# Kernel optimization log

Hardware: AMD Instinct MI355X
Metric: run time of the kernel (lower is better)

The kernel has to match this reference:

```python
import jax, jax.numpy as jnp
import numpy as np

NUM_HEADS = 8


def _mab(Q, K, Wq, bq, Wk, bk, Wv, bv, Wo, bo):
    # MAB with ln=False, dropout=0 (eval). Scale is sqrt(dim_V), matching source.
    B, Lq, _ = Q.shape
    Lk = K.shape[1]
    Dv = Wq.shape[1]
    dh = Dv // NUM_HEADS
    q = (Q @ Wq + bq).reshape(B, Lq, NUM_HEADS, dh).transpose(0, 2, 1, 3)
    k = (K @ Wk + bk).reshape(B, Lk, NUM_HEADS, dh).transpose(0, 2, 1, 3)
    v = (K @ Wv + bv).reshape(B, Lk, NUM_HEADS, dh).transpose(0, 2, 1, 3)
    A = jax.nn.softmax(jnp.einsum('bhqd,bhkd->bhqk', q, k) / jnp.sqrt(jnp.float32(Dv)), axis=-1)
    O = (q + jnp.einsum('bhqk,bhkd->bhqd', A, v)).transpose(0, 2, 1, 3).reshape(B, Lq, Dv)
    return O + jax.nn.relu(O @ Wo + bo)


def _forward(x, adj, gin_W, gin_b, geW1, geb1, geW2, geb2,
             gnW1, gnb1, gnW2, gnb2, goW, gob, S,
             mWq, mbq, mWk, mbk, mWv, mbv, mWo, mbo, finW, finb):
    B, V, T, D = x.shape
    Hd = gin_W.shape[1]
    # --- GNN encoder (adj path) ---
    h = x.reshape(B, V, T * D) @ gin_W + gin_b            # [B,V,H]
    # edge_mlp first linear on cat([h_i,h_j]) == h@Wi (row) + h@Wj (col); avoids 2H concat
    Wi, Wj = geW1[:Hd], geW1[Hd:]
    pre = (h @ Wi)[:, :, None, :] + (h @ Wj)[:, None, :, :] + geb1   # [B,V,V,H]
    e = jax.nn.relu(jax.nn.relu(pre) @ geW2 + geb2)       # [B,V,V,H]
    agg = jnp.einsum('bijh,bij->bih', e, adj)             # mask * sum over j, fused
    node = jax.nn.relu(jax.nn.relu(agg @ gnW1 + gnb1) @ gnW2 + gnb2)
    enc = node @ goW + gob                                # [B,V,H]
    # --- decoder: PMA + SAB + SAB + Linear ---
    o = _mab(jnp.broadcast_to(S, (B,) + S.shape[1:]), enc,
             mWq[0], mbq[0], mWk[0], mbk[0], mWv[0], mbv[0], mWo[0], mbo[0])
    o = _mab(o, o, mWq[1], mbq[1], mWk[1], mbk[1], mWv[1], mbv[1], mWo[1], mbo[1])
    o = _mab(o, o, mWq[2], mbq[2], mWk[2], mbk[2], mWv[2], mbv[2], mWo[2], mbo[2])
    out = o @ finW + finb                                 # [B,num_slots,T*OD]
    return out.reshape(B, S.shape[1], T, finW.shape[1] // T)


def setup_inputs() -> dict:
    key = jax.random.key(0)
    ks = jax.random.split(key, 16)
    B, V, T, D = 4, 256, 12, 4
    H, NS, OD = 256, 16, 32

    def w(k, shape, s=0.02):
        return s * jax.random.normal(k, shape, jnp.float32)

    return {
        'x': jax.random.normal(ks[0], (B, V, T, D), jnp.float32),
        'adj': (jax.random.uniform(ks[1], (B, V, V)) > 0.5).astype(jnp.float32),
        'gin_W': w(ks[2], (T * D, H)), 'gin_b': jnp.zeros((H,), jnp.float32),
        'geW1': w(ks[3], (2 * H, H)), 'geb1': jnp.zeros((H,), jnp.float32),
        'geW2': w(ks[4], (H, H)), 'geb2': jnp.zeros((H,), jnp.float32),
        'gnW1': w(ks[5], (H, H)), 'gnb1': jnp.zeros((H,), jnp.float32),
        'gnW2': w(ks[6], (H, H)), 'gnb2': jnp.zeros((H,), jnp.float32),
        'goW': w(ks[7], (H, H)), 'gob': jnp.zeros((H,), jnp.float32),
        'S': w(ks[8], (1, NS, H), 0.05),
        'mWq': w(ks[9], (3, H, H)), 'mbq': jnp.zeros((3, H), jnp.float32),
        'mWk': w(ks[10], (3, H, H)), 'mbk': jnp.zeros((3, H), jnp.float32),
        'mWv': w(ks[11], (3, H, H)), 'mbv': jnp.zeros((3, H), jnp.float32),
        'mWo': w(ks[12], (3, H, H)), 'mbo': jnp.zeros((3, H), jnp.float32),
        'finW': w(ks[13], (H, T * OD)), 'finb': jnp.zeros((T * OD,), jnp.float32),
    }


def reference(x, adj, gin_W, gin_b, geW1, geb1, geW2, geb2,
              gnW1, gnb1, gnW2, gnb2, goW, gob, S,
              mWq, mbq, mWk, mbk, mWv, mbv, mWo, mbo, finW, finb):
    return _forward(x, adj, gin_W, gin_b, geW1, geb1, geW2, geb2,
                    gnW1, gnb1, gnW2, gnb2, goW, gob, S,
                    mWq, mbq, mWk, mbk, mWv, mbv, mWo, mbo, finW, finb)
```

## Files before the change

### kernel.cpp

```cpp
#include <hip/hip_runtime.h>
#include <hip/hip_bf16.h>

typedef unsigned short u16;
typedef __bf16 bf8v __attribute__((ext_vector_type(8)));
typedef float f4v __attribute__((ext_vector_type(4)));

__device__ __forceinline__ float b2f(u16 v) {
  union { unsigned u; float f; } x; x.u = ((unsigned)v) << 16; return x.f;
}
__device__ __forceinline__ u16 f2b(float f) {
  union { float f; unsigned u; } x; x.f = f;
  unsigned r = (x.u + 0x7FFFu + ((x.u >> 16) & 1u)) >> 16;
  return (u16)r;
}
__device__ __forceinline__ unsigned pkbf(float a, float b) {
  union { __hip_bfloat162 h; unsigned u; } c;
  c.h = __float22bfloat162_rn(make_float2(a, b));
  return c.u;
}
__device__ __forceinline__ void up2(unsigned u, float& lo, float& hi) {
  union { unsigned x; float f; } a, b;
  a.x = u << 16; b.x = u & 0xffff0000u; lo = a.f; hi = b.f;
}

#define NFRAG 18

struct PreArgs {
  const float* fsrc[NFRAG];
  u16* fdst[NFRAG];
  int fstride[NFRAG];
  int fbase[NFRAG + 1];
  int fragTiles, hBase, prepBid, q1Bid;
  const float *x, *ginW, *ginb;
  u16* h_bf;
  const float *mbk, *mbv, *mbq, *S, *mWq;
  float *bkv0, *bqkv1, *bqkv2;
  u16* q1b;
};

__global__ __launch_bounds__(256) void k_pre(PreArgs a) {
  __shared__ __align__(16) char smem[27648];
  const int bid = blockIdx.x, t = threadIdx.x;

  if (bid < a.fragTiles) {
    u16* ld = (u16*)smem;
    int j = 0;
    while (j + 1 < NFRAG && a.fbase[j + 1] <= bid) j++;
    const int localT = bid - a.fbase[j];
    const float* src = a.fsrc[j];
    const int Ns = a.fstride[j];
    const int n0 = localT * 16;
    {
      const float* s = src + (size_t)t * Ns + n0;
      const float4 v0 = ((const float4*)s)[0], v1 = ((const float4*)s)[1];
      const float4 v2 = ((const float4*)s)[2], v3 = ((const float4*)s)[3];
      unsigned* row = (unsigned*)(ld + t * 20);
      row[0] = pkbf(v0.x, v0.y); row[1] = pkbf(v0.z, v0.w);
      row[2] = pkbf(v1.x, v1.y); row[3] = pkbf(v1.z, v1.w);
      row[4] = pkbf(v2.x, v2.y); row[5] = pkbf(v2.z, v2.w);
      row[6] = pkbf(v3.x, v3.y); row[7] = pkbf(v3.z, v3.w);
    }
    __syncthreads();
    u16* dst = a.fdst[j] + (size_t)localT * 4096;
#pragma unroll
    for (int s2 = 0; s2 < 2; s2++) {
      const int o = t * 2 + s2, kt = o >> 6, lane = o & 63;
      const int nlo = lane & 15, bk = kt * 32 + ((lane >> 4) << 3);
      union { u16 h[8]; uint4 q; } pk;
#pragma unroll
      for (int j2 = 0; j2 < 8; j2++) pk.h[j2] = ld[(bk + j2) * 20 + nlo];
      *(uint4*)(dst + (size_t)(kt * 64 + lane) * 8) = pk.q;
    }
    return;
  }
  if (bid < a.prepBid) {
    float (*xs)[48] = (float (*)[48])(smem + 10240);
    const int row0 = (bid - a.hBase) * 4;
    if (t < 192) {
      const int rr = t / 48, k = t % 48;
      xs[rr][k] = a.x[(size_t)(row0 + rr) * 48 + k];
    }
    __syncthreads();
    const float bias = a.ginb[t];
    float acc[4] = {bias, bias, bias, bias};
    for (int k = 0; k < 48; k++) {
      const float w = a.ginW[(size_t)k * 256 + t];
#pragma unroll
      for (int rr = 0; rr < 4; rr++) acc[rr] += xs[rr][k] * w;
    }
#pragma unroll
    for (int rr = 0; rr < 4; rr++) a.h_bf[(size_t)(row0 + rr) * 256 + t] = f2b(acc[rr]);
    return;
  }
  if (bid == a.prepBid) {
    a.bkv0[t] = a.mbk[t]; a.bkv0[256 + t] = a.mbv[t];
    a.bqkv1[t] = a.mbq[256 + t]; a.bqkv1[256 + t] = a.mbk[256 + t]; a.bqkv1[512 + t] = a.mbv[256 + t];
    a.bqkv2[t] = a.mbq[512 + t]; a.bqkv2[256 + t] = a.mbk[512 + t]; a.bqkv2[512 + t] = a.mbv[512 + t];
    return;
  }
  if (bid == a.q1Bid) {
    float* Ss = (float*)(smem + 11264);
    for (int idx = t; idx < 4096; idx += 256) Ss[idx] = a.S[idx];
    __syncthreads();
    float acc[16];
#pragma unroll
    for (int r = 0; r < 16; r++) acc[r] = 0.f;
    for (int k = 0; k < 256; k++) {
      const float w = a.mWq[(size_t)k * 256 + t];
#pragma unroll
      for (int r = 0; r < 16; r++) acc[r] += Ss[r * 256 + k] * w;
    }
    const float bq = a.mbq[t];
#pragma unroll
    for (int r = 0; r < 16; r++) a.q1b[r * 256 + t] = f2b(acc[r] + bq);
    return;
  }
}

__global__ __launch_bounds__(256) void k_wiwj(
    const u16* __restrict__ h, const u16* __restrict__ frag,
    float* __restrict__ hWiF, u16* __restrict__ hWjB) {
  __shared__ __align__(16) u16 As[64 * 264];
  const int t = threadIdx.x, lane = t & 63, wv = t >> 6;
  const int m0 = blockIdx.x * 64, n0 = blockIdx.y * 128;
  {
    const int row = t >> 2, ch = t & 3;
#pragma unroll
    for (int s = 0; s < 8; s++)
      *(uint4*)(As + row * 264 + ch * 64 + s * 8) =
          *(const uint4*)(h + (size_t)(m0 + row) * 256 + ch * 64 + s * 8);
  }
  __syncthreads();
  f4v acc[4][2];
#pragma unroll
  for (int mt = 0; mt < 4; mt++)
#pragma unroll
    for (int nt = 0; nt < 2; nt++) acc[mt][nt] = (f4v){0.f, 0.f, 0.f, 0.f};
  const int Tw = (n0 >> 4) + wv * 2;
#pragma unroll
  for (int kt = 0; kt < 8; kt++) {
    bf8v af[4], bf[2];
#pragma unroll
    for (int mt = 0; mt < 4; mt++)
      af[mt] = *(const bf8v*)(As + (mt * 16 + (lane & 15)) * 264 + kt * 32 + ((lane >> 4) << 3));
#pragma unroll
    for (int nt = 0; nt < 2; nt++)
      bf[nt] = *(const bf8v*)(frag + ((size_t)((Tw + nt) * 8 + kt) * 64 + lane) * 8);
#pragma unroll
    for (int mt = 0; mt < 4; mt++)
#pragma unroll
      for (int nt = 0; nt < 2; nt++)
        acc[mt][nt] = __builtin_amdgcn_mfma_f32_16x16x32_bf16(af[mt], bf[nt], acc[mt][nt], 0, 0, 0);
  }
#pragma unroll
  for (int mt = 0; mt < 4; mt++)
#pragma unroll
    for (int nt = 0; nt < 2; nt++) {
      const int n = n0 + wv * 32 + nt * 16 + (lane & 15);
      const int mb = m0 + mt * 16 + ((lane >> 4) << 2);
#pragma unroll
      for (int r = 0; r < 4; r++) {
        if (n < 256)
          hWiF[(size_t)(mb + r) * 256 + n] = acc[mt][nt][r];
        else
          hWjB[(size_t)(mb + r) * 256 + (n - 256)] = f2b(acc[mt][nt][r]);
      }
    }
}

__global__ __launch_bounds__(256, 2) void k_edge(
    const float* __restrict__ hWiF, const u16* __restrict__ hWjB,
    const float* __restrict__ adj, const float* __restrict__ geb1,
    const u16* __restrict__ fragW2, const float* __restrict__ geb2,
    u16* __restrict__ aggB) {
  __shared__ __align__(16) u16 As[64 * 280];
  __shared__ float hi[256];
  __shared__ int jlist[256];
  __shared__ int cnt;
  const int t = threadIdx.x, lane = t & 63, wv = t >> 6;
  const int b = blockIdx.x >> 8, i = blockIdx.x & 255;
  if (t == 0) cnt = 0;
  __syncthreads();
  {
    const float a = adj[(size_t)(b * 256 + i) * 256 + t];
    hi[t] = hWiF[(size_t)(b * 256 + i) * 256 + t] + geb1[t];
    if (a != 0.f) { const int p = atomicAdd(&cnt, 1); jlist[p] = t; }
  }
  __syncthreads();
  const int nact = cnt;
  if (nact == 0) {
    if (lane < 16) {
#pragma unroll
      for (int nt = 0; nt < 4; nt++)
        aggB[(size_t)(b * 256 + i) * 256 + wv * 64 + nt * 16 + lane] = 0;
    }
    return;
  }
  const int nch = (nact + 63) >> 6;
  float bias2[4];
#pragma unroll
  for (int nt = 0; nt < 4; nt++) bias2[nt] = geb2[wv * 64 + nt * 16 + (lane & 15)];
  float aggAcc[4] = {0.f, 0.f, 0.f, 0.f};
  const u16* fw = fragW2 + lane * 8;

  for (int c = 0; c < nch; c++) {
    const int rows = min(64, nact - c * 64);
    {
      const int r = t >> 2, q = t & 3;
      const bool valid = (r < rows);
      const int j = valid ? jlist[c * 64 + r] : jlist[0];
      const uint4* s4 = (const uint4*)(hWjB + (size_t)(b * 256 + j) * 256 + q * 64);
      u16* dstrow = As + r * 280 + q * 72;
#pragma unroll
      for (int ii = 0; ii < 8; ii++) {
        const uint4 v = s4[ii];
        const int k = q * 64 + ii * 8;
        float f0, f1, f2, f3, f4, f5, f6, f7;
        up2(v.x, f0, f1); up2(v.y, f2, f3); up2(v.z, f4, f5); up2(v.w, f6, f7);
        uint4 qd;
        qd.x = pkbf(fmaxf(f0 + hi[k + 0], 0.f), fmaxf(f1 + hi[k + 1], 0.f));
        qd.y = pkbf(fmaxf(f2 + hi[k + 2], 0.f), fmaxf(f3 + hi[k + 3], 0.f));
        qd.z = pkbf(fmaxf(f4 + hi[k + 4], 0.f), fmaxf(f5 + hi[k + 5], 0.f));
        qd.w = pkbf(fmaxf(f6 + hi[k + 6], 0.f), fmaxf(f7 + hi[k + 7], 0.f));
        *(uint4*)(dstrow + ii * 8) = qd;
      }
    }
    __syncthreads();
    f4v acc[4][4];
#pragma unroll
    for (int jt = 0; jt < 4; jt++)
#pragma unroll
      for (int nt = 0; nt < 4; nt++) acc[jt][nt] = (f4v){0.f, 0.f, 0.f, 0.f};
    bf8v bcur[4];
#pragma unroll
    for (int nt = 0; nt < 4; nt++)
      bcur[nt] = *(const bf8v*)(fw + (size_t)((wv * 4 + nt) * 8 + 0) * 512);
#pragma unroll
    for (int kt = 0; kt < 8; kt++) {
      bf8v bnxt[4];
      if (kt < 7) {
#pragma unroll
        for (int nt = 0; nt < 4; nt++)
          bnxt[nt] = *(const bf8v*)(fw + (size_t)((wv * 4 + nt) * 8 + kt + 1) * 512);
      }
      bf8v af[4];
      const int coff = (kt >> 1) * 72 + (kt & 1) * 32 + ((lane >> 4) << 3);
#pragma unroll
      for (int jt = 0; jt < 4; jt++)
        af[jt] = *(const bf8v*)(As + (jt * 16 + (lane & 15)) * 280 + coff);
#pragma unroll
      for (int nt = 0; nt < 4; nt++)
#pragma unroll
        for (int jt = 0; jt < 4; jt++)
          acc[jt][nt] = __builtin_amdgcn_mfma_f32_16x16x32_bf16(af[jt], bcur[nt], acc[jt][nt], 0, 0, 0);
      if (kt < 7) {
#pragma unroll
        for (int nt = 0; nt < 4; nt++) bcur[nt] = bnxt[nt];
      }
    }
    const int rbase = (lane >> 4) * 4;
#pragma unroll
    for (int nt = 0; nt < 4; nt++) {
      float s = 0.f;
#pragma unroll
      for (int jt = 0; jt < 4; jt++) {
        const int r0 = jt * 16 + rbase;
#pragma unroll
        for (int r = 0; r < 4; r++) {
          const float e = fmaxf(acc[jt][nt][r] + bias2[nt], 0.f);
          s += (r0 + r < rows) ? e : 0.f;
        }
      }
      s += __shfl_xor(s, 16);
      s += __shfl_xor(s, 32);
      aggAcc[nt] += s;
    }
    __syncthreads();
  }
  if (lane < 16) {
#pragma unroll
    for (int nt = 0; nt < 4; nt++) {
      const int n = wv * 64 + nt * 16 + lane;
      aggB[(size_t)(b * 256 + i) * 256 + n] = f2b(aggAcc[nt]);
    }
  }
}


__device__ void g16(const u16* Al, const u16* __restrict__ frag,
                    const float* bias, int relu, u16* Ol, int t) {
  const int lane = t & 63, wv = t >> 6;
  f4v acc[2];
  acc[0] = (f4v){0.f, 0.f, 0.f, 0.f};
  acc[1] = (f4v){0.f, 0.f, 0.f, 0.f};
  const u16* abase = Al + (lane & 15) * 264 + ((lane >> 4) << 3);
  const u16* f0 = frag + ((size_t)((wv * 2 + 0) * 8) * 64 + lane) * 8;
  const u16* f1 = frag + ((size_t)((wv * 2 + 1) * 8) * 64 + lane) * 8;
  bf8v bc0 = *(const bf8v*)f0;
  bf8v bc1 = *(const bf8v*)f1;
#pragma unroll
  for (int kt = 0; kt < 8; kt++) {
    bf8v bn0, bn1;
    if (kt < 7) {
      bn0 = *(const bf8v*)(f0 + (size_t)(kt + 1) * 512);
      bn1 = *(const bf8v*)(f1 + (size_t)(kt + 1) * 512);
    }
    const bf8v af = *(const bf8v*)(abase + kt * 32);
    acc[0] = __builtin_amdgcn_mfma_f32_16x16x32_bf16(af, bc0, acc[0], 0, 0, 0);
    acc[1] = __builtin_amdgcn_mfma_f32_16x16x32_bf16(af, bc1, acc[1], 0, 0, 0);
    if (kt < 7) { bc0 = bn0; bc1 = bn1; }
  }
#pragma unroll
  for (int nt = 0; nt < 2; nt++) {
    const int col = (wv * 2 + nt) * 16 + (lane & 15);
    const float bv = bias[col];
#pragma unroll
    for (int r = 0; r < 4; r++) {
      const int row = ((lane >> 4) << 2) + r;
      float v = acc[nt][r] + bv;
      if (relu) v = fmaxf(v, 0.f);
      Ol[row * 264 + col] = f2b(v);
    }
  }
}

__device__ void g16kv(const u16* Al, const u16* __restrict__ frag,
                      const float* bias, u16* outG, int t) {
  const int lane = t & 63, wv = t >> 6;
  f4v acc[4];
#pragma unroll
  for (int nt = 0; nt < 4; nt++) acc[nt] = (f4v){0.f, 0.f, 0.f, 0.f};
  const u16* abase = Al + (lane & 15) * 264 + ((lane >> 4) << 3);
  const u16* fb[4];
#pragma unroll
  for (int nt = 0; nt < 4; nt++)
    fb[nt] = frag + ((size_t)((wv * 4 + nt) * 8) * 64 + lane) * 8;
  bf8v bc[4];
#pragma unroll
  for (int nt = 0; nt < 4; nt++) bc[nt] = *(const bf8v*)fb[nt];
#pragma unroll
  for (int kt = 0; kt < 8; kt++) {
    bf8v bn[4];
    if (kt < 7) {
#pragma unroll
      for (int nt = 0; nt < 4; nt++)
        bn[nt] = *(const bf8v*)(fb[nt] + (size_t)(kt + 1) * 512);
    }
    const bf8v af = *(const bf8v*)(abase + kt * 32);
#pragma unroll
    for (int nt = 0; nt < 4; nt++)
      acc[nt] = __builtin_amdgcn_mfma_f32_16x16x32_bf16(af, bc[nt], acc[nt], 0, 0, 0);
    if (kt < 7) {
#pragma unroll
      for (int nt = 0; nt < 4; nt++) bc[nt] = bn[nt];
    }
  }
#pragma unroll
  for (int nt = 0; nt < 4; nt++) {
    const int col = (wv * 4 + nt) * 16 + (lane & 15);
    const float bv = bias[col];
#pragma unroll
    for (int r = 0; r < 4; r++) {
      const int row = ((lane >> 4) << 2) + r;
      outG[(size_t)row * 512 + col] = f2b(acc[nt][r] + bv);
    }
  }
}

__device__ void attn_tile(const u16* __restrict__ qbuf,
                          const u16* __restrict__ kbuf, const u16* __restrict__ vbuf,
                          float* __restrict__ oF, u16* __restrict__ oB,
                          int b, int hd, float* qs, float* sc, float* vs, int t) {
  const int lane = t & 63, wv = t >> 6;
  const int Lk = 256;
  if (t < 64) {
    const int row = t >> 2, part = t & 3;
    const uint4 q4 = *(const uint4*)(qbuf + (size_t)row * 256 + hd * 32 + part * 8);
    float f0, f1, f2, f3, f4, f5, f6, f7;
    up2(q4.x, f0, f1); up2(q4.y, f2, f3); up2(q4.z, f4, f5); up2(q4.w, f6, f7);
    float4* d = (float4*)(qs + row * 32 + part * 8);
    d[0] = make_float4(f0, f1, f2, f3);
    d[1] = make_float4(f4, f5, f6, f7);
  }
  __syncthreads();
  {
    float kv[32];
    const uint4* kp = (const uint4*)(kbuf + (size_t)(b * Lk + t) * 512 + hd * 32);
#pragma unroll
    for (int c4 = 0; c4 < 4; c4++) {
      const uint4 k4 = kp[c4];
      up2(k4.x, kv[c4 * 8 + 0], kv[c4 * 8 + 1]);
      up2(k4.y, kv[c4 * 8 + 2], kv[c4 * 8 + 3]);
      up2(k4.z, kv[c4 * 8 + 4], kv[c4 * 8 + 5]);
      up2(k4.w, kv[c4 * 8 + 6], kv[c4 * 8 + 7]);
    }
    for (int r = 0; r < 16; r++) {
      float s = 0.f;
#pragma unroll
      for (int d = 0; d < 32; d++) s += qs[r * 32 + d] * kv[d];
      sc[r * 256 + t] = s * 0.0625f;
    }
  }
  __syncthreads();
  for (int r = wv * 4; r < wv * 4 + 4; r++) {
    float v[4];
    float mx = -1e30f;
#pragma unroll
    for (int q2 = 0; q2 < 4; q2++) {
      v[q2] = sc[r * 256 + lane + q2 * 64];
      mx = fmaxf(mx, v[q2]);
    }
    for (int off = 32; off; off >>= 1) mx = fmaxf(mx, __shfl_xor(mx, off));
    float sum = 0.f;
#pragma unroll
    for (int q2 = 0; q2 < 4; q2++) { v[q2] = __expf(v[q2] - mx); sum += v[q2]; }
    for (int off = 32; off; off >>= 1) sum += __shfl_xor(sum, off);
    const float inv = 1.f / sum;
#pragma unroll
    for (int q2 = 0; q2 < 4; q2++) sc[r * 256 + lane + q2 * 64] = v[q2] * inv;
  }
  __syncthreads();
  for (int u = t; u < 1024; u += 256) {
    const int row = u >> 2, part = u & 3;
    const uint4 v4 = *(const uint4*)(vbuf + (size_t)(b * Lk + row) * 512 + hd * 32 + part * 8);
    float f0, f1, f2, f3, f4, f5, f6, f7;
    up2(v4.x, f0, f1); up2(v4.y, f2, f3); up2(v4.z, f4, f5); up2(v4.w, f6, f7);
    float4* d = (float4*)(vs + row * 32 + part * 8);
    d[0] = make_float4(f0, f1, f2, f3);
    d[1] = make_float4(f4, f5, f6, f7);
  }
  __syncthreads();
  const int r0 = t >> 5, d = t & 31;
  float a0 = qs[r0 * 32 + d], a1 = qs[(r0 + 8) * 32 + d];
#pragma unroll 4
  for (int j = 0; j < Lk; j++) {
    const float vv = vs[j * 32 + d];
    a0 += sc[r0 * 256 + j] * vv;
    a1 += sc[(r0 + 8) * 256 + j] * vv;
  }
  const int c0 = hd * 32 + d;
  oF[(size_t)(b * 16 + r0) * 256 + c0] = a0;
  oB[(size_t)(b * 16 + r0) * 256 + c0] = f2b(a0);
  oF[(size_t)(b * 16 + r0 + 8) * 256 + c0] = a1;
  oB[(size_t)(b * 16 + r0 + 8) * 256 + c0] = f2b(a1);
}

__device__ void wprojG(const u16* __restrict__ o1b, const float* __restrict__ o1f,
                       const u16* __restrict__ frag, const float* __restrict__ bias,
                       u16* actL, float* residL, int b, int T, int lane) {
  f4v acc = (f4v){0.f, 0.f, 0.f, 0.f};
  const u16* abase = o1b + (size_t)(b * 16 + (lane & 15)) * 256 + ((lane >> 4) << 3);
  const u16* fbase = frag + ((size_t)(T * 8) * 64 + lane) * 8;
#pragma unroll
  for (int kt = 0; kt < 8; kt++)
    acc = __builtin_amdgcn_mfma_f32_16x16x32_bf16(*(const bf8v*)(abase + kt * 32),
                                                  *(const bf8v*)(fbase + (size_t)kt * 512), acc, 0, 0, 0);
  const int col = T * 16 + (lane & 15);
  const float bv = bias[col];
#pragma unroll
  for (int r = 0; r < 4; r++) {
    const int row = ((lane >> 4) << 2) + r;
    const float v = fmaxf(acc[r] + bv, 0.f) + o1f[(size_t)(b * 16 + row) * 256 + col];
    residL[row * 256 + col] = v;
    actL[row * 264 + col] = f2b(v);
  }
}

template <int NT>
__device__ __forceinline__ void wprojQn(
    const u16* actL, const u16* __restrict__ frag,
    const float* __restrict__ bias, u16* qkvL, int T0, int lane) {
  f4v acc[NT];
#pragma unroll
  for (int nt = 0; nt < NT; nt++) acc[nt] = (f4v){0.f, 0.f, 0.f, 0.f};
  const u16* abase = actL + (lane & 15) * 264 + ((lane >> 4) << 3);
#pragma unroll
  for (int kt = 0; kt < 8; kt++) {
    const bf8v af = *(const bf8v*)(abase + kt * 32);
#pragma unroll
    for (int nt = 0; nt < NT; nt++) {
      const bf8v bf = *(const bf8v*)(frag + ((size_t)((T0 + nt) * 8 + kt) * 64 + lane) * 8);
      acc[nt] = __builtin_amdgcn_mfma_f32_16x16x32_bf16(af, bf, acc[nt], 0, 0, 0);
    }
  }
#pragma unroll
  for (int nt = 0; nt < NT; nt++) {
    const int col = (T0 + nt) * 16 + (lane & 15);
    const float bv = bias[col];
#pragma unroll
    for (int r = 0; r < 4; r++) {
      const int row = ((lane >> 4) << 2) + r;
      qkvL[row * 776 + col] = f2b(acc[nt][r] + bv);
    }
  }
}

__device__ void wprojR(const u16* actIn, const u16* __restrict__ frag,
                       const float* __restrict__ bias, u16* actOut, float* residL,
                       int T, int lane) {
  f4v acc = (f4v){0.f, 0.f, 0.f, 0.f};
  const u16* abase = actIn + (lane & 15) * 264 + ((lane >> 4) << 3);
  const u16* fbase = frag + ((size_t)(T * 8) * 64 + lane) * 8;
#pragma unroll
  for (int kt = 0; kt < 8; kt++)
    acc = __builtin_amdgcn_mfma_f32_16x16x32_bf16(*(const bf8v*)(abase + kt * 32),
                                                  *(const bf8v*)(fbase + (size_t)kt * 512), acc, 0, 0, 0);
  const int col = T * 16 + (lane & 15);
  const float bv = bias[col];
#pragma unroll
  for (int r = 0; r < 4; r++) {
    const int row = ((lane >> 4) << 2) + r;
    const float v = fmaxf(acc[r] + bv, 0.f) + residL[row * 256 + col];
    residL[row * 256 + col] = v;
    actOut[row * 264 + col] = f2b(v);
  }
}

__device__ void wprojF(const u16* actL, const u16* __restrict__ frag,
                       const float* __restrict__ bias, float* __restrict__ outG,
                       int T, int lane) {
  f4v acc = (f4v){0.f, 0.f, 0.f, 0.f};
  const u16* abase = actL + (lane & 15) * 264 + ((lane >> 4) << 3);
  const u16* fbase = frag + ((size_t)(T * 8) * 64 + lane) * 8;
#pragma unroll
  for (int kt = 0; kt < 8; kt++)
    acc = __builtin_amdgcn_mfma_f32_16x16x32_bf16(*(const bf8v*)(abase + kt * 32),
                                                  *(const bf8v*)(fbase + (size_t)kt * 512), acc, 0, 0, 0);
  const int col = T * 16 + (lane & 15);
  const float bv = bias[col];
#pragma unroll
  for (int r = 0; r < 4; r++) {
    const int row = ((lane >> 4) << 2) + r;
    outG[(size_t)row * 384 + col] = acc[r] + bv;
  }
}

__device__ void attnB(const u16* qkvL, float* residL, u16* actOut, float* ps,
                      int hd, int lane) {
  const int r = lane & 15, cg = lane >> 4;
  float qv[32];
  {
    const uint4* qp = (const uint4*)(qkvL + r * 776 + hd * 32);
#pragma unroll
    for (int c4 = 0; c4 < 4; c4++) {
      const uint4 q4 = qp[c4];
      up2(q4.x, qv[c4 * 8 + 0], qv[c4 * 8 + 1]);
      up2(q4.y, qv[c4 * 8 + 2], qv[c4 * 8 + 3]);
      up2(q4.z, qv[c4 * 8 + 4], qv[c4 * 8 + 5]);
      up2(q4.w, qv[c4 * 8 + 6], qv[c4 * 8 + 7]);
    }
  }
  float p[4];
#pragma unroll
  for (int c = 0; c < 4; c++) {
    const int cc = cg * 4 + c;
    const uint4* kp = (const uint4*)(qkvL + cc * 776 + 256 + hd * 32);
    float s = 0.f;
#pragma unroll
    for (int c4 = 0; c4 < 4; c4++) {
      const uint4 k4 = kp[c4];
      float k0, k1;
      up2(k4.x, k0, k1); s += qv[c4 * 8 + 0] * k0 + qv[c4 * 8 + 1] * k1;
      up2(k4.y, k0, k1); s += qv[c4 * 8 + 2] * k0 + qv[c4 * 8 + 3] * k1;
      up2(k4.z, k0, k1); s += qv[c4 * 8 + 4] * k0 + qv[c4 * 8 + 5] * k1;
      up2(k4.w, k0, k1); s += qv[c4 * 8 + 6] * k0 + qv[c4 * 8 + 7] * k1;
    }
    p[c] = s * 0.0625f;
  }
  float mx = fmaxf(fmaxf(p[0], p[1]), fmaxf(p[2], p[3]));
  mx = fmaxf(mx, __shfl_xor(mx, 16));
  mx = fmaxf(mx, __shfl_xor(mx, 32));
  float sum = 0.f;
#pragma unroll
  for (int c = 0; c < 4; c++) { p[c] = __expf(p[c] - mx); sum += p[c]; }
  sum += __shfl_xor(sum, 16);
  sum += __shfl_xor(sum, 32);
  const float inv = 1.f / sum;
#pragma unroll
  for (int c = 0; c < 4; c++) ps[r * 16 + cg * 4 + c] = p[c] * inv;
  float o[8];
#pragma unroll
  for (int j = 0; j < 8; j++) o[j] = qv[cg * 8 + j];
#pragma unroll
  for (int c = 0; c < 16; c++) {
    const float pv = ps[r * 16 + c];
    const uint4 v4 = *(const uint4*)(qkvL + c * 776 + 512 + hd * 32 + cg * 8);
    float v0, v1;
    up2(v4.x, v0, v1); o[0] += pv * v0; o[1] += pv * v1;
    up2(v4.y, v0, v1); o[2] += pv * v0; o[3] += pv * v1;
    up2(v4.z, v0, v1); o[4] += pv * v0; o[5] += pv * v1;
    up2(v4.w, v0, v1); o[6] += pv * v0; o[7] += pv * v1;
  }
  const int col0 = hd * 32 + cg * 8;
#pragma unroll
  for (int j = 0; j < 8; j++) residL[r * 256 + col0 + j] = o[j];
  unsigned* ob = (unsigned*)(actOut + r * 264 + col0);
  ob[0] = pkbf(o[0], o[1]); ob[1] = pkbf(o[2], o[3]);
  ob[2] = pkbf(o[4], o[5]); ob[3] = pkbf(o[6], o[7]);
}

struct TailArgs {
  const u16 *agg, *fGn1, *fGn2, *fGo, *fKV0, *fQKV1, *fQKV2, *fO0, *fO1, *fO2, *fFin, *q1b;
  const float *gnb1, *gnb2, *gob, *bkv0, *bqkv1, *bqkv2, *mbo, *finb;
  u16 *kv1, *o1b;
  float *o1f, *outF;
};

__global__ __launch_bounds__(512) void k_tail1(TailArgs a) {
  __shared__ __align__(16) u16 actA[16 * 264];
  __shared__ __align__(16) u16 actB[16 * 264];
  const int bid = blockIdx.x, t = threadIdx.x;
  const int r0 = bid * 16;
  {
    const int row = t >> 5, ch = t & 31;
    *(uint4*)(actA + row * 264 + ch * 8) =
        *(const uint4*)(a.agg + (size_t)(r0 + row) * 256 + ch * 8);
  }
  __syncthreads();
  g16(actA, a.fGn1, a.gnb1, 1, actB, t); __syncthreads();
  g16(actB, a.fGn2, a.gnb2, 1, actA, t); __syncthreads();
  g16(actA, a.fGo, a.gob, 0, actB, t); __syncthreads();
  g16kv(actB, a.fKV0, a.bkv0, a.kv1 + (size_t)r0 * 512, t);
}

__global__ __launch_bounds__(256) void k_tail2(TailArgs a) {
  __shared__ __align__(16) char smem[51200];
  float* qs = (float*)smem;
  float* sc = (float*)(smem + 2048);
  float* vs = (float*)(smem + 18432);
  attn_tile(a.q1b, a.kv1, a.kv1 + 256, a.o1f, a.o1b,
            (int)(blockIdx.x >> 3), (int)(blockIdx.x & 7), qs, sc, vs, (int)threadIdx.x);
}

__global__ __launch_bounds__(1024, 1) void k_tailB(TailArgs a) {
  __shared__ __align__(16) char smem[58112];
  const int t = threadIdx.x, lane = t & 63, w = t >> 6;
  const int b = blockIdx.x;
  u16* act0 = (u16*)smem;
  u16* act1 = (u16*)(smem + 8448);
  u16* qkvL = (u16*)(smem + 16896);
  float* residL = (float*)(smem + 41728);
  float* psL = (float*)smem;

  wprojG(a.o1b, a.o1f, a.fO0, a.mbo, act0, residL, b, w, lane);
  __syncthreads();
  wprojQn<3>(act0, a.fQKV1, a.bqkv1, qkvL, w * 3, lane);
  __syncthreads();
  if (w < 8) attnB(qkvL, residL, act1, psL + w * 256, w, lane);
  __syncthreads();
  wprojR(act1, a.fO1, a.mbo + 256, act0, residL, w, lane);
  __syncthreads();
  wprojQn<3>(act0, a.fQKV2, a.bqkv2, qkvL, w * 3, lane);
  __syncthreads();
  if (w < 8) attnB(qkvL, residL, act1, psL + w * 256, w, lane);
  __syncthreads();
  wprojR(act1, a.fO2, a.mbo + 512, act0, residL, w, lane);
  __syncthreads();
  for (int T = w; T < 24; T += 16)
    wprojF(act0, a.fFin, a.finb, a.outF + (size_t)b * 16 * 384, T, lane);
}

extern "C" void kernel_launch(void* const* d_in, const int* in_sizes, int n_in,
                              void* d_out, int out_size, void* d_ws, size_t ws_size,
                              hipStream_t stream) {
  const float* x    = (const float*)d_in[0];
  const float* adj  = (const float*)d_in[1];
  const float* ginW = (const float*)d_in[2];
  const float* ginb = (const float*)d_in[3];
  const float* geW1 = (const float*)d_in[4];
  const float* geb1 = (const float*)d_in[5];
  const float* geW2 = (const float*)d_in[6];
  const float* geb2 = (const float*)d_in[7];
  const float* gnW1 = (const float*)d_in[8];
  const float* gnb1 = (const float*)d_in[9];
  const float* gnW2 = (const float*)d_in[10];
  const float* gnb2 = (const float*)d_in[11];
  const float* goW  = (const float*)d_in[12];
  const float* gob  = (const float*)d_in[13];
  const float* S    = (const float*)d_in[14];
  const float* mWq  = (const float*)d_in[15];
  const float* mbq  = (const float*)d_in[16];
  const float* mWk  = (const float*)d_in[17];
  const float* mbk  = (const float*)d_in[18];
  const float* mWv  = (const float*)d_in[19];
  const float* mbv  = (const float*)d_in[20];
  const float* mWo  = (const float*)d_in[21];
  const float* mbo  = (const float*)d_in[22];
  const float* finW = (const float*)d_in[23];
  const float* finb = (const float*)d_in[24];
  (void)in_sizes; (void)n_in; (void)out_size; (void)ws_size;

  char* wp = (char*)d_ws;
  size_t off = 0;
  auto alloc = [&](size_t bytes) -> char* {
    char* p = wp + off;
    off += (bytes + 255) & ~(size_t)255;
    return p;
  };
  u16* h_bf     = (u16*)alloc(1024 * 256 * 2);
  float* hWiF   = (float*)alloc((size_t)1024 * 256 * 4);
  u16* hWjB     = (u16*)alloc(1024 * 256 * 2);
  u16* fWiWj    = (u16*)alloc(512 * 256 * 2);
  u16* fW2      = (u16*)alloc(256 * 256 * 2);
  u16* fGn1     = (u16*)alloc(256 * 256 * 2);
  u16* fGn2     = (u16*)alloc(256 * 256 * 2);
  u16* fGo      = (u16*)alloc(256 * 256 * 2);
  u16* fKV0     = (u16*)alloc(512 * 256 * 2);
  u16* fQKV1    = (u16*)alloc(768 * 256 * 2);
  u16* fQKV2    = (u16*)alloc(768 * 256 * 2);
  u16* fO0      = (u16*)alloc(256 * 256 * 2);
  u16* fO1      = (u16*)alloc(256 * 256 * 2);
  u16* fO2      = (u16*)alloc(256 * 256 * 2);
  u16* fFin     = (u16*)alloc(384 * 256 * 2);
  float* bkv0   = (float*)alloc(512 * 4);
  float* bqkv1  = (float*)alloc(768 * 4);
  float* bqkv2  = (float*)alloc(768 * 4);
  u16* q1b      = (u16*)alloc(16 * 256 * 2);
  u16* agg_b    = (u16*)alloc(1024 * 256 * 2);
  u16* kv1      = (u16*)alloc(1024 * 512 * 2);
  float* o1f    = (float*)alloc(64 * 256 * 4);
  u16* o1b      = (u16*)alloc(64 * 256 * 2);

  PreArgs P{};
  int nj = 0, tiles = 0;
  auto addF = [&](const float* s, int stride, u16* d, int nT) {
    P.fsrc[nj] = s; P.fdst[nj] = d; P.fstride[nj] = stride; P.fbase[nj] = tiles;
    tiles += nT; nj++;
  };
  addF(geW1, 256, fWiWj, 16);
  addF(geW1 + 65536, 256, fWiWj + 16 * 4096, 16);
  addF(geW2, 256, fW2, 16);
  addF(gnW1, 256, fGn1, 16);
  addF(gnW2, 256, fGn2, 16);
  addF(goW, 256, fGo, 16);
  addF(mWk, 256, fKV0, 16);
  addF(mWv, 256, fKV0 + 16 * 4096, 16);
  addF(mWq + 65536, 256, fQKV1, 16);
  addF(mWk + 65536, 256, fQKV1 + 16 * 4096, 16);
  addF(mWv + 65536, 256, fQKV1 + 32 * 4096, 16);
  addF(mWq + 131072, 256, fQKV2, 16);
  addF(mWk + 131072, 256, fQKV2 + 16 * 4096, 16);
  addF(mWv + 131072, 256, fQKV2 + 32 * 4096, 16);
  addF(mWo, 256, fO0, 16);
  addF(mWo + 65536, 256, fO1, 16);
  addF(mWo + 131072, 256, fO2, 16);
  addF(finW, 384, fFin, 24);
  P.fbase[nj] = tiles;
  P.fragTiles = tiles;
  P.hBase = tiles;
  P.prepBid = tiles + 256;
  P.q1Bid = tiles + 257;
  P.x = x; P.ginW = ginW; P.ginb = ginb; P.h_bf = h_bf;
  P.mbk = mbk; P.mbv = mbv; P.mbq = mbq; P.S = S; P.mWq = mWq;
  P.bkv0 = bkv0; P.bqkv1 = bqkv1; P.bqkv2 = bqkv2; P.q1b = q1b;

  TailArgs T{};
  T.agg = agg_b; T.fGn1 = fGn1; T.fGn2 = fGn2; T.fGo = fGo; T.fKV0 = fKV0;
  T.fQKV1 = fQKV1; T.fQKV2 = fQKV2; T.fO0 = fO0; T.fO1 = fO1; T.fO2 = fO2;
  T.fFin = fFin; T.q1b = q1b;
  T.gnb1 = gnb1; T.gnb2 = gnb2; T.gob = gob;
  T.bkv0 = bkv0; T.bqkv1 = bqkv1; T.bqkv2 = bqkv2; T.mbo = mbo; T.finb = finb;
  T.kv1 = kv1; T.o1b = o1b; T.o1f = o1f; T.outF = (float*)d_out;

  k_pre<<<dim3(tiles + 258), dim3(256), 0, stream>>>(P);
  k_wiwj<<<dim3(16, 4), dim3(256), 0, stream>>>(h_bf, fWiWj, hWiF, hWjB);
  k_edge<<<dim3(1024), dim3(256), 0, stream>>>(hWiF, hWjB, adj, geb1, fW2, geb2, agg_b);
  k_tail1<<<dim3(64), dim3(512), 0, stream>>>(T);
  k_tail2<<<dim3(32), dim3(256), 0, stream>>>(T);
  k_tailB<<<dim3(4), dim3(1024), 0, stream>>>(T);
}
```

Baseline: 220.8 us.

## Fuse three tail kernels into one persistent kernel with grid barriers

Merges the tail1, tail2 and tailB kernels into a single 64-block, 1024-thread kernel. Software grid barriers on a global atomic counter, reset in k_pre, separate the phases. Each phase's work is redistributed across 16 waves: single-tile GEMMs per wave and one attention row per wave. This removes two kernel launch gaps and their tail latency, but adds atomic spin barriers, relies on all 64 blocks being co-resident, and leaves most blocks idle in the later phases.

```diff
diff --git a/kernel.cpp b/kernel.cpp
--- a/kernel.cpp
+++ b/kernel.cpp
@@ -24,6 +24,7 @@
 }
 
 #define NFRAG 18
+#define TBLK 64
 
 struct PreArgs {
   const float* fsrc[NFRAG];
@@ -36,6 +37,7 @@
   const float *mbk, *mbv, *mbq, *S, *mWq;
   float *bkv0, *bqkv1, *bqkv2;
   u16* q1b;
+  int* bar;
 };
 
 __global__ __launch_bounds__(256) void k_pre(PreArgs a) {
@@ -93,6 +95,7 @@
     return;
   }
   if (bid == a.prepBid) {
+    if (t < 64) a.bar[t] = 0;
     a.bkv0[t] = a.mbk[t]; a.bkv0[256 + t] = a.mbv[t];
     a.bqkv1[t] = a.mbq[256 + t]; a.bqkv1[256 + t] = a.mbk[256 + t]; a.bqkv1[512 + t] = a.mbv[256 + t];
     a.bqkv2[t] = a.mbq[512 + t]; a.bqkv2[256 + t] = a.mbk[512 + t]; a.bqkv2[512 + t] = a.mbv[512 + t];
@@ -286,16 +289,55 @@
   }
 }
 
-
-__device__ void g16(const u16* Al, const u16* __restrict__ frag,
-                    const float* bias, int relu, u16* Ol, int t) {
-  const int lane = t & 63, wv = t >> 6;
+__device__ __forceinline__ void gridbar(int* cnt, int gen) {
+  __syncthreads();
+  if (threadIdx.x == 0) {
+    __hip_atomic_fetch_add(cnt, 1, __ATOMIC_RELEASE, __HIP_MEMORY_SCOPE_AGENT);
+    int it = 0;
+    while (__hip_atomic_load(cnt, __ATOMIC_ACQUIRE, __HIP_MEMORY_SCOPE_AGENT) < TBLK * gen) {
+      __builtin_amdgcn_s_sleep(8);
+      if (((++it) & 255) == 0)
+        __hip_atomic_fetch_add(cnt, 0, __ATOMIC_ACQ_REL, __HIP_MEMORY_SCOPE_AGENT);
+    }
+  }
+  __syncthreads();
+}
+
+__device__ void g16w(const u16* Al, const u16* __restrict__ frag,
+                     const float* bias, int relu, u16* Ol, int t) {
+  const int lane = t & 63, w = t >> 6;
+  f4v acc = (f4v){0.f, 0.f, 0.f, 0.f};
+  const u16* abase = Al + (lane & 15) * 264 + ((lane >> 4) << 3);
+  const u16* fb = frag + ((size_t)(w * 8) * 64 + lane) * 8;
+  bf8v bc = *(const bf8v*)fb;
+#pragma unroll
+  for (int kt = 0; kt < 8; kt++) {
+    bf8v bn;
+    if (kt < 7) bn = *(const bf8v*)(fb + (size_t)(kt + 1) * 512);
+    const bf8v af = *(const bf8v*)(abase + kt * 32);
+    acc = __builtin_amdgcn_mfma_f32_16x16x32_bf16(af, bc, acc, 0, 0, 0);
+    if (kt < 7) bc = bn;
+  }
+  const int col = w * 16 + (lane & 15);
+  const float bv = bias[col];
+#pragma unroll
+  for (int r = 0; r < 4; r++) {
+    const int row = ((lane >> 4) << 2) + r;
+    float v = acc[r] + bv;
+    if (relu) v = fmaxf(v, 0.f);
+    Ol[row * 264 + col] = f2b(v);
+  }
+}
+
+__device__ void g16kv2(const u16* Al, const u16* __restrict__ frag,
+                       const float* bias, u16* outG, int t) {
+  const int lane = t & 63, w = t >> 6;
   f4v acc[2];
   acc[0] = (f4v){0.f, 0.f, 0.f, 0.f};
   acc[1] = (f4v){0.f, 0.f, 0.f, 0.f};
   const u16* abase = Al + (lane & 15) * 264 + ((lane >> 4) << 3);
-  const u16* f0 = frag + ((size_t)((wv * 2 + 0) * 8) * 64 + lane) * 8;
-  const u16* f1 = frag + ((size_t)((wv * 2 + 1) * 8) * 64 + lane) * 8;
+  const u16* f0 = frag + ((size_t)((w * 2 + 0) * 8) * 64 + lane) * 8;
+  const u16* f1 = frag + ((size_t)((w * 2 + 1) * 8) * 64 + lane) * 8;
   bf8v bc0 = *(const bf8v*)f0;
   bf8v bc1 = *(const bf8v*)f1;
 #pragma unroll
@@ -312,52 +354,7 @@
   }
 #pragma unroll
   for (int nt = 0; nt < 2; nt++) {
-    const int col = (wv * 2 + nt) * 16 + (lane & 15);
-    const float bv = bias[col];
-#pragma unroll
-    for (int r = 0; r < 4; r++) {
-      const int row = ((lane >> 4) << 2) + r;
-      float v = acc[nt][r] + bv;
-      if (relu) v = fmaxf(v, 0.f);
-      Ol[row * 264 + col] = f2b(v);
-    }
-  }
-}
-
-__device__ void g16kv(const u16* Al, const u16* __restrict__ frag,
-                      const float* bias, u16* outG, int t) {
-  const int lane = t & 63, wv = t >> 6;
-  f4v acc[4];
-#pragma unroll
-  for (int nt = 0; nt < 4; nt++) acc[nt] = (f4v){0.f, 0.f, 0.f, 0.f};
-  const u16* abase = Al + (lane & 15) * 264 + ((lane >> 4) << 3);
-  const u16* fb[4];
-#pragma unroll
-  for (int nt = 0; nt < 4; nt++)
-    fb[nt] = frag + ((size_t)((wv * 4 + nt) * 8) * 64 + lane) * 8;
-  bf8v bc[4];
-#pragma unroll
-  for (int nt = 0; nt < 4; nt++) bc[nt] = *(const bf8v*)fb[nt];
-#pragma unroll
-  for (int kt = 0; kt < 8; kt++) {
-    bf8v bn[4];
-    if (kt < 7) {
-#pragma unroll
-      for (int nt = 0; nt < 4; nt++)
-        bn[nt] = *(const bf8v*)(fb[nt] + (size_t)(kt + 1) * 512);
-    }
-    const bf8v af = *(const bf8v*)(abase + kt * 32);
-#pragma unroll
-    for (int nt = 0; nt < 4; nt++)
-      acc[nt] = __builtin_amdgcn_mfma_f32_16x16x32_bf16(af, bc[nt], acc[nt], 0, 0, 0);
-    if (kt < 7) {
-#pragma unroll
-      for (int nt = 0; nt < 4; nt++) bc[nt] = bn[nt];
-    }
-  }
-#pragma unroll
-  for (int nt = 0; nt < 4; nt++) {
-    const int col = (wv * 4 + nt) * 16 + (lane & 15);
+    const int col = (w * 2 + nt) * 16 + (lane & 15);
     const float bv = bias[col];
 #pragma unroll
     for (int r = 0; r < 4; r++) {
@@ -367,11 +364,11 @@
   }
 }
 
-__device__ void attn_tile(const u16* __restrict__ qbuf,
-                          const u16* __restrict__ kbuf, const u16* __restrict__ vbuf,
-                          float* __restrict__ oF, u16* __restrict__ oB,
-                          int b, int hd, float* qs, float* sc, float* vs, int t) {
-  const int lane = t & 63, wv = t >> 6;
+__device__ void attn_tile_1024(const u16* __restrict__ qbuf,
+                               const u16* __restrict__ kbuf, const u16* __restrict__ vbuf,
+                               float* __restrict__ oF, u16* __restrict__ oB,
+                               int b, int hd, float* qs, float* sc, float* vs, int t) {
+  const int lane = t & 63, w = t >> 6;
   const int Lk = 256;
   if (t < 64) {
     const int row = t >> 2, part = t & 3;
@@ -383,7 +380,7 @@
     d[1] = make_float4(f4, f5, f6, f7);
   }
   __syncthreads();
-  {
+  if (t < 256) {
     float kv[32];
     const uint4* kp = (const uint4*)(kbuf + (size_t)(b * Lk + t) * 512 + hd * 32);
 #pragma unroll
@@ -402,7 +399,8 @@
     }
   }
   __syncthreads();
-  for (int r = wv * 4; r < wv * 4 + 4; r++) {
+  {
+    const int r = w;
     float v[4];
     float mx = -1e30f;
 #pragma unroll
@@ -420,8 +418,8 @@
     for (int q2 = 0; q2 < 4; q2++) sc[r * 256 + lane + q2 * 64] = v[q2] * inv;
   }
   __syncthreads();
-  for (int u = t; u < 1024; u += 256) {
-    const int row = u >> 2, part = u & 3;
+  {
+    const int row = t >> 2, part = t & 3;
     const uint4 v4 = *(const uint4*)(vbuf + (size_t)(b * Lk + row) * 512 + hd * 32 + part * 8);
     float f0, f1, f2, f3, f4, f5, f6, f7;
     up2(v4.x, f0, f1); up2(v4.y, f2, f3); up2(v4.z, f4, f5); up2(v4.w, f6, f7);
@@ -430,19 +428,15 @@
     d[1] = make_float4(f4, f5, f6, f7);
   }
   __syncthreads();
-  const int r0 = t >> 5, d = t & 31;
-  float a0 = qs[r0 * 32 + d], a1 = qs[(r0 + 8) * 32 + d];
+  if (t < 512) {
+    const int r0 = t >> 5, d = t & 31;
+    float a0 = qs[r0 * 32 + d];
 #pragma unroll 4
-  for (int j = 0; j < Lk; j++) {
-    const float vv = vs[j * 32 + d];
-    a0 += sc[r0 * 256 + j] * vv;
-    a1 += sc[(r0 + 8) * 256 + j] * vv;
-  }
-  const int c0 = hd * 32 + d;
-  oF[(size_t)(b * 16 + r0) * 256 + c0] = a0;
-  oB[(size_t)(b * 16 + r0) * 256 + c0] = f2b(a0);
-  oF[(size_t)(b * 16 + r0 + 8) * 256 + c0] = a1;
-  oB[(size_t)(b * 16 + r0 + 8) * 256 + c0] = f2b(a1);
+    for (int j = 0; j < Lk; j++) a0 += sc[r0 * 256 + j] * vs[j * 32 + d];
+    const int c0 = hd * 32 + d;
+    oF[(size_t)(b * 16 + r0) * 256 + c0] = a0;
+    oB[(size_t)(b * 16 + r0) * 256 + c0] = f2b(a0);
+  }
 }
 
 __device__ void wprojG(const u16* __restrict__ o1b, const float* __restrict__ o1f,
@@ -604,60 +598,64 @@
   const float *gnb1, *gnb2, *gob, *bkv0, *bqkv1, *bqkv2, *mbo, *finb;
   u16 *kv1, *o1b;
   float *o1f, *outF;
+  int* bar;
 };
 
-__global__ __launch_bounds__(512) void k_tail1(TailArgs a) {
-  __shared__ __align__(16) u16 actA[16 * 264];
-  __shared__ __align__(16) u16 actB[16 * 264];
+__global__ __launch_bounds__(1024) void k_tailM(TailArgs a) {
+  __shared__ __align__(16) char smem[58112];
   const int bid = blockIdx.x, t = threadIdx.x;
-  const int r0 = bid * 16;
+  const int lane = t & 63, w = t >> 6;
+
   {
-    const int row = t >> 5, ch = t & 31;
-    *(uint4*)(actA + row * 264 + ch * 8) =
-        *(const uint4*)(a.agg + (size_t)(r0 + row) * 256 + ch * 8);
-  }
-  __syncthreads();
-  g16(actA, a.fGn1, a.gnb1, 1, actB, t); __syncthreads();
-  g16(actB, a.fGn2, a.gnb2, 1, actA, t); __syncthreads();
-  g16(actA, a.fGo, a.gob, 0, actB, t); __syncthreads();
-  g16kv(actB, a.fKV0, a.bkv0, a.kv1 + (size_t)r0 * 512, t);
-}
-
-__global__ __launch_bounds__(256) void k_tail2(TailArgs a) {
-  __shared__ __align__(16) char smem[51200];
-  float* qs = (float*)smem;
-  float* sc = (float*)(smem + 2048);
-  float* vs = (float*)(smem + 18432);
-  attn_tile(a.q1b, a.kv1, a.kv1 + 256, a.o1f, a.o1b,
-            (int)(blockIdx.x >> 3), (int)(blockIdx.x & 7), qs, sc, vs, (int)threadIdx.x);
-}
-
-__global__ __launch_bounds__(1024, 1) void k_tailB(TailArgs a) {
-  __shared__ __align__(16) char smem[58112];
-  const int t = threadIdx.x, lane = t & 63, w = t >> 6;
-  const int b = blockIdx.x;
-  u16* act0 = (u16*)smem;
-  u16* act1 = (u16*)(smem + 8448);
-  u16* qkvL = (u16*)(smem + 16896);
-  float* residL = (float*)(smem + 41728);
-  float* psL = (float*)smem;
-
-  wprojG(a.o1b, a.o1f, a.fO0, a.mbo, act0, residL, b, w, lane);
-  __syncthreads();
-  wprojQn<3>(act0, a.fQKV1, a.bqkv1, qkvL, w * 3, lane);
-  __syncthreads();
-  if (w < 8) attnB(qkvL, residL, act1, psL + w * 256, w, lane);
-  __syncthreads();
-  wprojR(act1, a.fO1, a.mbo + 256, act0, residL, w, lane);
-  __syncthreads();
-  wprojQn<3>(act0, a.fQKV2, a.bqkv2, qkvL, w * 3, lane);
-  __syncthreads();
-  if (w < 8) attnB(qkvL, residL, act1, psL + w * 256, w, lane);
-  __syncthreads();
-  wprojR(act1, a.fO2, a.mbo + 512, act0, residL, w, lane);
-  __syncthreads();
-  for (int T = w; T < 24; T += 16)
-    wprojF(act0, a.fFin, a.finb, a.outF + (size_t)b * 16 * 384, T, lane);
+    u16* actA = (u16*)smem;
+    u16* actB = (u16*)(smem + 8448);
+    const int r0 = bid * 16;
+    if (t < 512) {
+      const int row = t >> 5, ch = t & 31;
+      *(uint4*)(actA + row * 264 + ch * 8) =
+          *(const uint4*)(a.agg + (size_t)(r0 + row) * 256 + ch * 8);
+    }
+    __syncthreads();
+    g16w(actA, a.fGn1, a.gnb1, 1, actB, t); __syncthreads();
+    g16w(actB, a.fGn2, a.gnb2, 1, actA, t); __syncthreads();
+    g16w(actA, a.fGo, a.gob, 0, actB, t); __syncthreads();
+    g16kv2(actB, a.fKV0, a.bkv0, a.kv1 + (size_t)r0 * 512, t);
+  }
+  gridbar(a.bar, 1);
+  if (bid < 32) {
+    float* qs = (float*)smem;
+    float* sc = (float*)(smem + 2048);
+    float* vs = (float*)(smem + 18432);
+    attn_tile_1024(a.q1b, a.kv1, a.kv1 + 256, a.o1f, a.o1b,
+                   bid >> 3, bid & 7, qs, sc, vs, t);
+  }
+  gridbar(a.bar, 2);
+  if (bid >= 4) return;
+  {
+    const int b = bid;
+    u16* act0 = (u16*)smem;
+    u16* act1 = (u16*)(smem + 8448);
+    u16* qkvL = (u16*)(smem + 16896);
+    float* residL = (float*)(smem + 41728);
+    float* psL = (float*)smem;
+    __syncthreads();
+    wprojG(a.o1b, a.o1f, a.fO0, a.mbo, act0, residL, b, w, lane);
+    __syncthreads();
+    wprojQn<3>(act0, a.fQKV1, a.bqkv1, qkvL, w * 3, lane);
+    __syncthreads();
+    if (w < 8) attnB(qkvL, residL, act1, psL + w * 256, w, lane);
+    __syncthreads();
+    wprojR(act1, a.fO1, a.mbo + 256, act0, residL, w, lane);
+    __syncthreads();
+    wprojQn<3>(act0, a.fQKV2, a.bqkv2, qkvL, w * 3, lane);
+    __syncthreads();
+    if (w < 8) attnB(qkvL, residL, act1, psL + w * 256, w, lane);
+    __syncthreads();
+    wprojR(act1, a.fO2, a.mbo + 512, act0, residL, w, lane);
+    __syncthreads();
+    for (int T = w; T < 24; T += 16)
+      wprojF(act0, a.fFin, a.finb, a.outF + (size_t)b * 16 * 384, T, lane);
+  }
 }
 
 extern "C" void kernel_launch(void* const* d_in, const int* in_sizes, int n_in,
@@ -720,6 +718,7 @@
   u16* kv1      = (u16*)alloc(1024 * 512 * 2);
   float* o1f    = (float*)alloc(64 * 256 * 4);
   u16* o1b      = (u16*)alloc(64 * 256 * 2);
+  int* bar      = (int*)alloc(256);
 
   PreArgs P{};
   int nj = 0, tiles = 0;
@@ -753,6 +752,7 @@
   P.x = x; P.ginW = ginW; P.ginb = ginb; P.h_bf = h_bf;
   P.mbk = mbk; P.mbv = mbv; P.mbq = mbq; P.S = S; P.mWq = mWq;
   P.bkv0 = bkv0; P.bqkv1 = bqkv1; P.bqkv2 = bqkv2; P.q1b = q1b;
+  P.bar = bar;
 
   TailArgs T{};
   T.agg = agg_b; T.fGn1 = fGn1; T.fGn2 = fGn2; T.fGo = fGo; T.fKV0 = fKV0;
@@ -761,11 +761,10 @@
   T.gnb1 = gnb1; T.gnb2 = gnb2; T.gob = gob;
   T.bkv0 = bkv0; T.bqkv1 = bqkv1; T.bqkv2 = bqkv2; T.mbo = mbo; T.finb = finb;
   T.kv1 = kv1; T.o1b = o1b; T.o1f = o1f; T.outF = (float*)d_out;
+  T.bar = bar;
 
   k_pre<<<dim3(tiles + 258), dim3(256), 0, stream>>>(P);
   k_wiwj<<<dim3(16, 4), dim3(256), 0, stream>>>(h_bf, fWiWj, hWiF, hWjB);
   k_edge<<<dim3(1024), dim3(256), 0, stream>>>(hWiF, hWjB, adj, geb1, fW2, geb2, agg_b);
-  k_tail1<<<dim3(64), dim3(512), 0, stream>>>(T);
-  k_tail2<<<dim3(32), dim3(256), 0, stream>>>(T);
-  k_tailB<<<dim3(4), dim3(1024), 0, stream>>>(T);
-}
+  k_tailM<<<dim3(TBLK), dim3(1024), 0, stream>>>(T);
+}
```

After: 222.8 us. About the same (+0.9%).
